# Optimization experiments

Measured on AMD Instinct MI355X. Metric: run time of the kernel, lower is better.

Reference implementation:

```python
import jax, jax.numpy as jnp
import numpy as np
from jax import lax

N_P = 0.5      # module_cfg.n_p
CUTOFF = 0.3   # module_cfg.cutoff


def setup_inputs() -> dict:
    key = jax.random.key(0)
    k1, k2, k3, k4 = jax.random.split(key, 4)
    h = jax.random.normal(k1, (1, 8192, 256), jnp.float32)
    pos = jax.random.normal(k2, (8192, 3), jnp.float32)
    W = jax.random.normal(k3, (256, 256), jnp.float32) / 16.0  # ~ Linear init scale
    b = jax.random.normal(k4, (256,), jnp.float32) * 0.01
    return {"h": h, "pos": pos, "W": W, "b": b}


def fps_indices(pos, k, select=0):
    """Farthest point sampling; returns the k selected indices in ascending
    index order (matching torch boolean-mask indexing pos[selected])."""
    n = pos.shape[0]
    selected = jnp.zeros(n, dtype=bool).at[select].set(True)
    d = jnp.linalg.norm(pos - pos[select], axis=-1)  # (N,) euclidean, as torch.pairwise_distance
    d = jnp.where(selected, -jnp.inf, d)

    def body(i, carry):
        sel, dist = carry
        new = jnp.argmax(dist)
        sel = sel.at[new].set(True)
        dist = jnp.minimum(dist, jnp.linalg.norm(pos - pos[new], axis=-1))
        dist = jnp.where(sel, -jnp.inf, dist)
        return sel, dist

    sel, _ = lax.fori_loop(0, k - 1, body, (selected, d))
    return jnp.nonzero(sel, size=k)[0]  # exactly k True entries, sorted


def reference(h, pos, W, b):
    B, num_res, c_s = h.shape
    n_nodes = int(num_res * N_P)  # num_res * n_p // 1

    idx = fps_indices(pos, n_nodes)          # (n_nodes,)
    new_node_pos = pos[idx]                  # (n_nodes, 3)

    # torch.cdist(pos, new_node_pos, p=3): Minkowski p=3 distance
    diff = jnp.abs(pos[:, None, :] - new_node_pos[None, :, :])  # (N, n_nodes, 3)
    dist = jnp.cbrt(jnp.sum(diff ** 3, axis=-1))                 # (N, n_nodes)

    # sparse membership mask (fixed-shape equivalent of the nonzero edge list)
    mask = dist < CUTOFF                      # (N, n_nodes) bool

    # sparse gather-matmul: aggregate residue features into each sampled node
    agg = jnp.einsum('nm,bnc->bmc', mask.astype(h.dtype), h)     # (B, n_nodes, c_s)
    new_node_embed = agg @ W.T + b            # nn.Linear(c_s, c_s)
    return new_node_embed, new_node_pos, mask
```

## Files before the change

### kernel.cpp

```cpp
#include <hip/hip_runtime.h>
#include <hip/hip_bf16.h>
#include <cmath>

#define FPS_N 8192
#define FPS_K 4096
#define CS    256
#define FT    1024
#define PPT   8
#define NEGINF (-__builtin_inff())

__device__ __forceinline__ float p3sum(float x, float y, float z,
                                       float nx, float ny, float nz) {
  float dx = fabsf(__fsub_rn(x, nx));
  float dy = fabsf(__fsub_rn(y, ny));
  float dz = fabsf(__fsub_rn(z, nz));
  float cx = __fmul_rn(__fmul_rn(dx, dx), dx);
  float cy = __fmul_rn(__fmul_rn(dy, dy), dy);
  float cz = __fmul_rn(__fmul_rn(dz, dz), dz);
  return __fadd_rn(__fadd_rn(cx, cy), cz);
}

__device__ __forceinline__ float eucl2(float x, float y, float z,
                                       float nx, float ny, float nz) {
  float dx = __fsub_rn(x, nx);
  float dy = __fsub_rn(y, ny);
  float dz = __fsub_rn(z, nz);
  return __fadd_rn(__fadd_rn(__fmul_rn(dx, dx), __fmul_rn(dy, dy)),
                   __fmul_rn(dz, dz));
}

template<int CTRL>
__device__ __forceinline__ void dpp_sel2(float& v, int& k) {
  int nv = __builtin_amdgcn_update_dpp(__float_as_int(v), __float_as_int(v), CTRL, 0xF, 0xF, false);
  int nk = __builtin_amdgcn_update_dpp(k, k, CTRL, 0xF, 0xF, false);
  float fv = __int_as_float(nv);
  bool t = (fv > v) || (fv == v && nk < k);
  v = t ? fv : v;
  k = t ? nk : k;
}

template<int CTRL>
__device__ __forceinline__ void dpp_sel5(float& v, int& k, float& x, float& y, float& z) {
  int nv = __builtin_amdgcn_update_dpp(__float_as_int(v), __float_as_int(v), CTRL, 0xF, 0xF, false);
  int nk = __builtin_amdgcn_update_dpp(k, k, CTRL, 0xF, 0xF, false);
  int nx = __builtin_amdgcn_update_dpp(__float_as_int(x), __float_as_int(x), CTRL, 0xF, 0xF, false);
  int ny = __builtin_amdgcn_update_dpp(__float_as_int(y), __float_as_int(y), CTRL, 0xF, 0xF, false);
  int nz = __builtin_amdgcn_update_dpp(__float_as_int(z), __float_as_int(z), CTRL, 0xF, 0xF, false);
  float fv = __int_as_float(nv);
  bool t = (fv > v) || (fv == v && nk < k);
  v = t ? fv : v;
  k = t ? nk : k;
  x = t ? __int_as_float(nx) : x;
  y = t ? __int_as_float(ny) : y;
  z = t ? __int_as_float(nz) : z;
}

__global__ __launch_bounds__(FT) void bin_kernel(const float* __restrict__ pos,
                                                 float* __restrict__ pos_s,
                                                 int* __restrict__ ids_s) {
  __shared__ int hist[4096];
  __shared__ int part[FT];
  const int tid = threadIdx.x;
#pragma unroll
  for (int i = 0; i < 4; ++i) hist[tid * 4 + i] = 0;
  __syncthreads();

  float qx[PPT], qy[PPT], qz[PPT];
  int cell[PPT];
  {
    const float4* p4 = (const float4*)pos + tid * 6;
    float4 a0 = p4[0], a1 = p4[1], a2 = p4[2], a3 = p4[3], a4 = p4[4], a5 = p4[5];
    qx[0]=a0.x; qy[0]=a0.y; qz[0]=a0.z;
    qx[1]=a0.w; qy[1]=a1.x; qz[1]=a1.y;
    qx[2]=a1.z; qy[2]=a1.w; qz[2]=a2.x;
    qx[3]=a2.y; qy[3]=a2.z; qz[3]=a2.w;
    qx[4]=a3.x; qy[4]=a3.y; qz[4]=a3.z;
    qx[5]=a3.w; qy[5]=a4.x; qz[5]=a4.y;
    qx[6]=a4.z; qy[6]=a4.w; qz[6]=a5.x;
    qx[7]=a5.y; qy[7]=a5.z; qz[7]=a5.w;
  }
#pragma unroll
  for (int j = 0; j < PPT; ++j) {
    int ix = min(max((int)floorf((qx[j] + 4.0f) * 2.0f), 0), 15);
    int iy = min(max((int)floorf((qy[j] + 4.0f) * 2.0f), 0), 15);
    int iz = min(max((int)floorf((qz[j] + 4.0f) * 2.0f), 0), 15);
    int m = 0;
#pragma unroll
    for (int b = 0; b < 4; ++b)
      m |= (((ix >> b) & 1) << (3 * b)) | (((iy >> b) & 1) << (3 * b + 1)) |
           (((iz >> b) & 1) << (3 * b + 2));
    cell[j] = m;
    atomicAdd(&hist[m], 1);
  }
  __syncthreads();
  int h0 = hist[tid * 4], h1 = hist[tid * 4 + 1], h2 = hist[tid * 4 + 2], h3 = hist[tid * 4 + 3];
  int s = h0 + h1 + h2 + h3;
  part[tid] = s;
  __syncthreads();
  for (int off = 1; off < FT; off <<= 1) {
    int u = (tid >= off) ? part[tid - off] : 0;
    __syncthreads();
    part[tid] += u;
    __syncthreads();
  }
  int base = part[tid] - s;
  hist[tid * 4 + 0] = base;
  hist[tid * 4 + 1] = base + h0;
  hist[tid * 4 + 2] = base + h0 + h1;
  hist[tid * 4 + 3] = base + h0 + h1 + h2;
  __syncthreads();
#pragma unroll
  for (int j = 0; j < PPT; ++j) {
    int slot = atomicAdd(&hist[cell[j]], 1);
    pos_s[slot * 3 + 0] = qx[j];
    pos_s[slot * 3 + 1] = qy[j];
    pos_s[slot * 3 + 2] = qz[j];
    ids_s[slot] = tid * PPT + j;
  }
}

#define KEYOF(j) (((((idp[(j) >> 1] >> (((j) & 1) * 16)) & 0xffff)) << 13) | (tid * PPT + (j)))
#define SELP(va, ka, vb, kb) { bool t_ = ((vb) > (va)) || ((vb) == (va) && (kb) < (ka)); \
                               va = t_ ? (vb) : (va); ka = t_ ? (kb) : (ka); }
#define RESCAN() { \
    float v0 = dd[0], v1 = dd[1], v2 = dd[2], v3 = dd[3]; \
    float v4 = dd[4], v5 = dd[5], v6 = dd[6], v7 = dd[7]; \
    int k0 = KEYOF(0), k1 = KEYOF(1), k2 = KEYOF(2), k3 = KEYOF(3); \
    int k4 = KEYOF(4), k5 = KEYOF(5), k6 = KEYOF(6), k7 = KEYOF(7); \
    SELP(v0, k0, v1, k1) SELP(v2, k2, v3, k3) SELP(v4, k4, v5, k5) SELP(v6, k6, v7, k7) \
    SELP(v0, k0, v2, k2) SELP(v4, k4, v6, k6) SELP(v0, k0, v4, k4) \
    bv = v0; bkey = k0; }

__global__ __launch_bounds__(FT) void fps_kernel(const float* __restrict__ pos,
                                                 const float* __restrict__ pos_s,
                                                 const int* __restrict__ ids_s,
                                                 float* __restrict__ pos_out) {
  __shared__ int sC[2][5][16];
  __shared__ unsigned char flag[FPS_N];
  __shared__ int sc[FT];
  const int tid = threadIdx.x, lane = tid & 63, wave = tid >> 6;

  { int* f4 = (int*)flag; f4[tid * 2] = 0; f4[tid * 2 + 1] = 0; }

  float x[PPT], y[PPT], z[PPT], d2[PPT], dd[PPT];
  int idp[PPT / 2];
  {
    const float4* p4 = (const float4*)pos_s + tid * 6;
    float4 a0 = p4[0], a1 = p4[1], a2 = p4[2], a3 = p4[3], a4 = p4[4], a5 = p4[5];
    x[0]=a0.x; y[0]=a0.y; z[0]=a0.z;
    x[1]=a0.w; y[1]=a1.x; z[1]=a1.y;
    x[2]=a1.z; y[2]=a1.w; z[2]=a2.x;
    x[3]=a2.y; y[3]=a2.z; z[3]=a2.w;
    x[4]=a3.x; y[4]=a3.y; z[4]=a3.z;
    x[5]=a3.w; y[5]=a4.x; z[5]=a4.y;
    x[6]=a4.z; y[6]=a4.w; z[6]=a5.x;
    x[7]=a5.y; y[7]=a5.z; z[7]=a5.w;
    const int4* i4 = (const int4*)ids_s + tid * 2;
    int4 b0 = i4[0], b1 = i4[1];
    idp[0] = (b0.x & 0xffff) | (b0.y << 16);
    idp[1] = (b0.z & 0xffff) | (b0.w << 16);
    idp[2] = (b1.x & 0xffff) | (b1.y << 16);
    idp[3] = (b1.z & 0xffff) | (b1.w << 16);
  }

  const float p0x = pos[0], p0y = pos[1], p0z = pos[2];
#pragma unroll
  for (int j = 0; j < PPT; ++j) {
    float s = eucl2(x[j], y[j], z[j], p0x, p0y, p0z);
    int oid = (idp[j >> 1] >> ((j & 1) * 16)) & 0xffff;
    if (oid == 0) { d2[j] = NEGINF; dd[j] = NEGINF; }
    else          { d2[j] = s;      dd[j] = sqrtf(s); }
  }
  float bnx = x[0], bny = y[0], bnz = z[0], bxx = x[0], bxy = y[0], bxz = z[0];
#pragma unroll
  for (int j = 1; j < PPT; ++j) {
    bnx = fminf(bnx, x[j]); bny = fminf(bny, y[j]); bnz = fminf(bnz, z[j]);
    bxx = fmaxf(bxx, x[j]); bxy = fmaxf(bxy, y[j]); bxz = fmaxf(bxz, z[j]);
  }
  if (tid == 0) flag[0] = 1;

  float bv; int bkey; bool chb;
  RESCAN();
  chb = false;
  {
    float rv = bv; int rk = bkey;
    dpp_sel2<0x111>(rv, rk); dpp_sel2<0x112>(rv, rk); dpp_sel2<0x114>(rv, rk);
    dpp_sel2<0x118>(rv, rk); dpp_sel2<0x142>(rv, rk); dpp_sel2<0x143>(rv, rk);
    int wkk = __builtin_amdgcn_readlane(rk, 63);
    if (bkey == wkk) {
      float sx = x[0], sy = y[0], sz = z[0];
#pragma unroll
      for (int j = 0; j < PPT; ++j)
        if (j == (bkey & 7)) { sx = x[j]; sy = y[j]; sz = z[j]; }
      sC[0][0][wave] = __float_as_int(bv);
      sC[0][1][wave] = bkey;
      sC[0][2][wave] = __float_as_int(sx);
      sC[0][3][wave] = __float_as_int(sy);
      sC[0][4][wave] = __float_as_int(sz);
    }
  }
  __syncthreads();

  for (int k = 0; k < FPS_K - 1; ++k) {
    const int p = k & 1, pn = p ^ 1;
    float gv = __int_as_float(sC[p][0][lane & 15]);
    int   gk = sC[p][1][lane & 15];
    float gx = __int_as_float(sC[p][2][lane & 15]);
    float gy = __int_as_float(sC[p][3][lane & 15]);
    float gz = __int_as_float(sC[p][4][lane & 15]);
    dpp_sel5<0xB1>(gv, gk, gx, gy, gz);
    dpp_sel5<0x4E>(gv, gk, gx, gy, gz);
    dpp_sel5<0x124>(gv, gk, gx, gy, gz);
    dpp_sel5<0x128>(gv, gk, gx, gy, gz);

    const int stor = gk & 8191;
    if ((stor >> 3) == tid) {
      const int jj = stor & 7;
#pragma unroll
      for (int j = 0; j < PPT; ++j)
        if (j == jj) { d2[j] = NEGINF; dd[j] = NEGINF; }
      chb = true;
    }
    if (tid == 0) flag[gk >> 13] = 1;

    float cx = fminf(fmaxf(gx, bnx), bxx);
    float cy = fminf(fmaxf(gy, bny), bxy);
    float cz = fminf(fmaxf(gz, bnz), bxz);
    float ddx = gx - cx, ddy = gy - cy, ddz = gz - cz;
    float bd2 = ddx * ddx + ddy * ddy + ddz * ddz;
    float tub = (bv == NEGINF) ? NEGINF : bv * bv;
    if (bd2 * 0.999f < tub) {
      unsigned cm = 0;
#pragma unroll
      for (int j = 0; j < PPT; ++j) {
        float s = eucl2(x[j], y[j], z[j], gx, gy, gz);
        if (s < d2[j]) { d2[j] = s; cm |= (1u << j); }
      }
      if (cm) {
#pragma unroll
        for (int j = 0; j < PPT; ++j)
          if ((cm >> j) & 1) dd[j] = sqrtf(d2[j]);
        if ((cm >> (bkey & 7)) & 1) chb = true;
      }
    }

    unsigned long long any = __ballot(chb ? 1 : 0);
    if (any) {
      if (chb) { RESCAN(); chb = false; }
      float rv = bv; int rk = bkey;
      dpp_sel2<0x111>(rv, rk); dpp_sel2<0x112>(rv, rk); dpp_sel2<0x114>(rv, rk);
      dpp_sel2<0x118>(rv, rk); dpp_sel2<0x142>(rv, rk); dpp_sel2<0x143>(rv, rk);
      int wkk = __builtin_amdgcn_readlane(rk, 63);
      if (bkey == wkk) {
        float sx = x[0], sy = y[0], sz = z[0];
#pragma unroll
        for (int j = 0; j < PPT; ++j)
          if (j == (bkey & 7)) { sx = x[j]; sy = y[j]; sz = z[j]; }
        sC[pn][0][wave] = __float_as_int(bv);
        sC[pn][1][wave] = bkey;
        sC[pn][2][wave] = __float_as_int(sx);
        sC[pn][3][wave] = __float_as_int(sy);
        sC[pn][4][wave] = __float_as_int(sz);
      }
    } else {
      if (lane < 5) sC[pn][lane][wave] = sC[p][lane][wave];
    }
    __syncthreads();
  }

  const int* fI = (const int*)flag;
  int w0 = fI[tid * 2], w1 = fI[tid * 2 + 1];
  int cnt = __popc(w0) + __popc(w1);
  sc[tid] = cnt;
  __syncthreads();
  for (int off = 1; off < FT; off <<= 1) {
    int u = (tid >= off) ? sc[tid - off] : 0;
    __syncthreads();
    sc[tid] += u;
    __syncthreads();
  }
  int r = sc[tid] - cnt;
#pragma unroll
  for (int j = 0; j < PPT; ++j) {
    int w = (j < 4) ? w0 : w1;
    if ((w >> ((j & 3) * 8)) & 1) {
      int oi = tid * PPT + j;
      pos_out[r * 3 + 0] = pos[oi * 3 + 0];
      pos_out[r * 3 + 1] = pos[oi * 3 + 1];
      pos_out[r * 3 + 2] = pos[oi * 3 + 2];
      ++r;
    }
  }
}

__global__ __launch_bounds__(256) void wt_kernel(const float* __restrict__ W,
                                                 float* __restrict__ WT) {
  int i = blockIdx.x * 256 + threadIdx.x;
  int c = i >> 8, cp = i & 255;
  WT[i] = W[cp * 256 + c];
}

__global__ __launch_bounds__(256) void agg_linear_kernel(
    const float* __restrict__ h, const float* __restrict__ pos,
    const float* __restrict__ nodepos, const float* __restrict__ WT,
    const float* __restrict__ bias, float* __restrict__ embed, float sb) {
  const int m = blockIdx.x;
  const int tid = threadIdx.x;
  const int lane = tid & 63, wave = tid >> 6;
  const float nx = nodepos[m * 3 + 0];
  const float ny = nodepos[m * 3 + 1];
  const float nz = nodepos[m * 3 + 2];
  const float4* h4 = (const float4*)h;

  float4 acc = make_float4(0.f, 0.f, 0.f, 0.f);
  const int base0 = wave * (FPS_N / 4);
  for (int base = base0; base < base0 + (FPS_N / 4); base += 64) {
    int n = base + lane;
    float px = pos[n * 3 + 0], py = pos[n * 3 + 1], pz = pos[n * 3 + 2];
    unsigned long long mb = __ballot((p3sum(px, py, pz, nx, ny, nz) <= sb) ? 1 : 0);
    while (mb) {
      int b = __ffsll(mb) - 1;
      mb &= (mb - 1);
      float4 hv = h4[(size_t)(base + b) * 64 + lane];
      acc.x += hv.x; acc.y += hv.y; acc.z += hv.z; acc.w += hv.w;
    }
  }

  __shared__ float lacc[4][256];
  lacc[wave][lane * 4 + 0] = acc.x;
  lacc[wave][lane * 4 + 1] = acc.y;
  lacc[wave][lane * 4 + 2] = acc.z;
  lacc[wave][lane * 4 + 3] = acc.w;
  __syncthreads();
  __shared__ float aggrow[256];
  float aggv = ((lacc[0][tid] + lacc[1][tid]) + lacc[2][tid]) + lacc[3][tid];
  aggrow[tid] = aggv;
  __syncthreads();

  float o = bias[tid];
#pragma unroll 8
  for (int c = 0; c < 256; ++c)
    o = fmaf(aggrow[c], WT[c * 256 + tid], o);
  embed[(size_t)m * 256 + tid] = o;
}

__global__ __launch_bounds__(256) void mask_kernel(const float* __restrict__ pos,
                                                   const float* __restrict__ nodepos,
                                                   float* __restrict__ maskout,
                                                   float sb) {
  int n  = blockIdx.y;
  int m0 = (blockIdx.x * 256 + threadIdx.x) * 4;
  float x = pos[n * 3 + 0], y = pos[n * 3 + 1], z = pos[n * 3 + 2];
  const float4* np4 = (const float4*)(nodepos + (size_t)m0 * 3);
  float4 a = np4[0], bq = np4[1], cq = np4[2];
  float4 r;
  r.x = (p3sum(x, y, z, a.x,  a.y,  a.z)  <= sb) ? 1.0f : 0.0f;
  r.y = (p3sum(x, y, z, a.w,  bq.x, bq.y) <= sb) ? 1.0f : 0.0f;
  r.z = (p3sum(x, y, z, bq.z, bq.w, cq.x) <= sb) ? 1.0f : 0.0f;
  r.w = (p3sum(x, y, z, cq.y, cq.z, cq.w) <= sb) ? 1.0f : 0.0f;
  *(float4*)(maskout + (size_t)n * FPS_K + m0) = r;
}

extern "C" void kernel_launch(void* const* d_in, const int* in_sizes, int n_in,
                              void* d_out, int out_size, void* d_ws, size_t ws_size,
                              hipStream_t stream) {
  (void)in_sizes; (void)n_in; (void)out_size; (void)d_ws; (void)ws_size;
  const float* h   = (const float*)d_in[0];
  const float* pos = (const float*)d_in[1];
  const float* W   = (const float*)d_in[2];
  const float* b   = (const float*)d_in[3];

  float* out     = (float*)d_out;
  float* embed   = out;
  float* pos_out = out + (size_t)FPS_K * CS;
  float* mask    = pos_out + (size_t)FPS_K * 3;
  float* WT      = mask;
  float* pos_s   = mask + (1 << 21);
  int*   ids_s   = (int*)(pos_s + 3 * FPS_N);

  const float  t    = 0.3f;
  const float  ulpv = nextafterf(t, 1.0f) - t;
  const double rmid = (double)t - (double)ulpv * 0.5;
  const double C    = rmid * rmid * rmid;
  float sb = (float)C;
  if (!((double)sb < C)) sb = nextafterf(sb, 0.0f);

  hipLaunchKernelGGL(bin_kernel, dim3(1), dim3(FT), 0, stream, pos, pos_s, ids_s);
  hipLaunchKernelGGL(fps_kernel, dim3(1), dim3(FT), 0, stream, pos, pos_s, ids_s, pos_out);
  hipLaunchKernelGGL(wt_kernel, dim3(256), dim3(256), 0, stream, W, WT);
  hipLaunchKernelGGL(agg_linear_kernel, dim3(FPS_K), dim3(256), 0, stream,
                     h, pos, pos_out, WT, b, embed, sb);
  hipLaunchKernelGGL(mask_kernel, dim3(4, FPS_N), dim3(256), 0, stream,
                     pos, pos_out, mask, sb);
}
```

Measured before the change: 7.559 ms.

## Batch multiple FPS selections per barrier using per-wave top-2 candidates

```diff
diff --git a/kernel.cpp b/kernel.cpp
--- a/kernel.cpp
+++ b/kernel.cpp
@@ -8,6 +8,7 @@
 #define FT    1024
 #define PPT   8
 #define NEGINF (-__builtin_inff())
+#define KMAX  0x7fffffff
 
 __device__ __forceinline__ float p3sum(float x, float y, float z,
                                        float nx, float ny, float nz) {
@@ -29,30 +30,39 @@
                    __fmul_rn(dz, dz));
 }
 
+#define LEXGT(va, ka, vb, kb) (((va) > (vb)) || ((va) == (vb) && ((ka) < (kb))))
+
 template<int CTRL>
-__device__ __forceinline__ void dpp_sel2(float& v, int& k) {
-  int nv = __builtin_amdgcn_update_dpp(__float_as_int(v), __float_as_int(v), CTRL, 0xF, 0xF, false);
-  int nk = __builtin_amdgcn_update_dpp(k, k, CTRL, 0xF, 0xF, false);
-  float fv = __int_as_float(nv);
-  bool t = (fv > v) || (fv == v && nk < k);
-  v = t ? fv : v;
-  k = t ? nk : k;
-}
-
+__device__ __forceinline__ int dppi(int a) {
+  return __builtin_amdgcn_update_dpp(a, a, CTRL, 0xF, 0xF, false);
+}
 template<int CTRL>
-__device__ __forceinline__ void dpp_sel5(float& v, int& k, float& x, float& y, float& z) {
-  int nv = __builtin_amdgcn_update_dpp(__float_as_int(v), __float_as_int(v), CTRL, 0xF, 0xF, false);
-  int nk = __builtin_amdgcn_update_dpp(k, k, CTRL, 0xF, 0xF, false);
-  int nx = __builtin_amdgcn_update_dpp(__float_as_int(x), __float_as_int(x), CTRL, 0xF, 0xF, false);
-  int ny = __builtin_amdgcn_update_dpp(__float_as_int(y), __float_as_int(y), CTRL, 0xF, 0xF, false);
-  int nz = __builtin_amdgcn_update_dpp(__float_as_int(z), __float_as_int(z), CTRL, 0xF, 0xF, false);
-  float fv = __int_as_float(nv);
-  bool t = (fv > v) || (fv == v && nk < k);
-  v = t ? fv : v;
-  k = t ? nk : k;
-  x = t ? __int_as_float(nx) : x;
-  y = t ? __int_as_float(ny) : y;
-  z = t ? __int_as_float(nz) : z;
+__device__ __forceinline__ float dppf(float a) {
+  return __int_as_float(__builtin_amdgcn_update_dpp(__float_as_int(a), __float_as_int(a), CTRL, 0xF, 0xF, false));
+}
+
+template<int CTRL>
+__device__ __forceinline__ void dpp_sel7(float& v, int& k, float& x, float& y,
+                                         float& z, float& v2, int& k2) {
+  float pv = dppf<CTRL>(v);  int pk = dppi<CTRL>(k);
+  float px = dppf<CTRL>(x);  float py = dppf<CTRL>(y);  float pz = dppf<CTRL>(z);
+  float pv2 = dppf<CTRL>(v2); int pk2 = dppi<CTRL>(k2);
+  bool t = LEXGT(pv, pk, v, k);
+  v = t ? pv : v;   k = t ? pk : k;
+  x = t ? px : x;   y = t ? py : y;   z = t ? pz : z;
+  v2 = t ? pv2 : v2; k2 = t ? pk2 : k2;
+}
+
+template<int CTRL>
+__device__ __forceinline__ void dpp_top2(float& v1, int& k1, float& v2, int& k2) {
+  float p1 = dppf<CTRL>(v1); int q1 = dppi<CTRL>(k1);
+  float p2 = dppf<CTRL>(v2); int q2 = dppi<CTRL>(k2);
+  bool t = LEXGT(p1, q1, v1, k1);
+  float lv = t ? v1 : p1; int lk = t ? k1 : q1;
+  float ov = t ? p2 : v2; int ok = t ? q2 : k2;
+  v1 = t ? p1 : v1; k1 = t ? q1 : k1;
+  bool u = LEXGT(lv, lk, ov, ok);
+  v2 = u ? lv : ov; k2 = u ? lk : ok;
 }
 
 __global__ __launch_bounds__(FT) void bin_kernel(const float* __restrict__ pos,
@@ -120,22 +130,57 @@
 }
 
 #define KEYOF(j) (((((idp[(j) >> 1] >> (((j) & 1) * 16)) & 0xffff)) << 13) | (tid * PPT + (j)))
-#define SELP(va, ka, vb, kb) { bool t_ = ((vb) > (va)) || ((vb) == (va) && (kb) < (ka)); \
-                               va = t_ ? (vb) : (va); ka = t_ ? (kb) : (ka); }
-#define RESCAN() { \
-    float v0 = dd[0], v1 = dd[1], v2 = dd[2], v3 = dd[3]; \
-    float v4 = dd[4], v5 = dd[5], v6 = dd[6], v7 = dd[7]; \
-    int k0 = KEYOF(0), k1 = KEYOF(1), k2 = KEYOF(2), k3 = KEYOF(3); \
-    int k4 = KEYOF(4), k5 = KEYOF(5), k6 = KEYOF(6), k7 = KEYOF(7); \
-    SELP(v0, k0, v1, k1) SELP(v2, k2, v3, k3) SELP(v4, k4, v5, k5) SELP(v6, k6, v7, k7) \
-    SELP(v0, k0, v2, k2) SELP(v4, k4, v6, k6) SELP(v0, k0, v4, k4) \
-    bv = v0; bkey = k0; }
+
+#define PAIR2(v1, k1, v2, k2, a, ka, b, kb) { bool t_ = LEXGT(b, kb, a, ka); \
+  v1 = t_ ? (b) : (a); k1 = t_ ? (kb) : (ka); v2 = t_ ? (a) : (b); k2 = t_ ? (ka) : (kb); }
+
+#define MERGE22(v1, k1, v2, k2, w1, l1, w2, l2) { \
+  bool t_ = LEXGT(w1, l1, v1, k1); \
+  float lv_ = t_ ? (v1) : (w1); int lk_ = t_ ? (k1) : (l1); \
+  float ov_ = t_ ? (w2) : (v2); int ok_ = t_ ? (l2) : (k2); \
+  v1 = t_ ? (w1) : (v1); k1 = t_ ? (l1) : (k1); \
+  bool u_ = LEXGT(lv_, lk_, ov_, ok_); \
+  v2 = u_ ? lv_ : ov_; k2 = u_ ? lk_ : ok_; }
+
+#define RESCAN2() { \
+  float A1, B1, C1, D1, A2, B2, C2, D2; int Ak, Bk, Ck, Dk, Ak2, Bk2, Ck2, Dk2; \
+  PAIR2(A1, Ak, A2, Ak2, dd[0], KEYOF(0), dd[1], KEYOF(1)) \
+  PAIR2(B1, Bk, B2, Bk2, dd[2], KEYOF(2), dd[3], KEYOF(3)) \
+  PAIR2(C1, Ck, C2, Ck2, dd[4], KEYOF(4), dd[5], KEYOF(5)) \
+  PAIR2(D1, Dk, D2, Dk2, dd[6], KEYOF(6), dd[7], KEYOF(7)) \
+  MERGE22(A1, Ak, A2, Ak2, B1, Bk, B2, Bk2) \
+  MERGE22(C1, Ck, C2, Ck2, D1, Dk, D2, Dk2) \
+  MERGE22(A1, Ak, A2, Ak2, C1, Ck, C2, Ck2) \
+  bv = A1; bkey = Ak; bv2 = A2; bk2 = Ak2; }
+
+#define WAVE_PUBLISH(sn) { \
+  float rv1 = bv; int rk1 = bkey; float rv2 = bv2; int rk2 = bk2; \
+  dpp_top2<0x111>(rv1, rk1, rv2, rk2); dpp_top2<0x112>(rv1, rk1, rv2, rk2); \
+  dpp_top2<0x114>(rv1, rk1, rv2, rk2); dpp_top2<0x118>(rv1, rk1, rv2, rk2); \
+  dpp_top2<0x142>(rv1, rk1, rv2, rk2); dpp_top2<0x143>(rv1, rk1, rv2, rk2); \
+  int wk1u = __builtin_amdgcn_readlane(rk1, 63); \
+  int wv2u = __builtin_amdgcn_readlane(__float_as_int(rv2), 63); \
+  int wk2u = __builtin_amdgcn_readlane(rk2, 63); \
+  if (bkey == wk1u) { \
+    const int jj_ = bkey & 7; \
+    float sx_ = x[0], sy_ = y[0], sz_ = z[0]; \
+    _Pragma("unroll") \
+    for (int j = 0; j < PPT; ++j) \
+      if (j == jj_) { sx_ = x[j]; sy_ = y[j]; sz_ = z[j]; } \
+    sC[sn][0][wave] = __float_as_int(bv); \
+    sC[sn][1][wave] = bkey; \
+    sC[sn][2][wave] = __float_as_int(sx_); \
+    sC[sn][3][wave] = __float_as_int(sy_); \
+    sC[sn][4][wave] = __float_as_int(sz_); \
+    sC[sn][5][wave] = wv2u; \
+    sC[sn][6][wave] = wk2u; \
+  } }
 
 __global__ __launch_bounds__(FT) void fps_kernel(const float* __restrict__ pos,
                                                  const float* __restrict__ pos_s,
                                                  const int* __restrict__ ids_s,
                                                  float* __restrict__ pos_out) {
-  __shared__ int sC[2][5][16];
+  __shared__ int sC[2][7][16];
   __shared__ unsigned char flag[FPS_N];
   __shared__ int sc[FT];
   const int tid = threadIdx.x, lane = tid & 63, wave = tid >> 6;
@@ -179,92 +224,111 @@
   }
   if (tid == 0) flag[0] = 1;
 
-  float bv; int bkey; bool chb;
-  RESCAN();
+  float bv, bv2; int bkey, bk2; bool chb;
+  RESCAN2();
   chb = false;
-  {
-    float rv = bv; int rk = bkey;
-    dpp_sel2<0x111>(rv, rk); dpp_sel2<0x112>(rv, rk); dpp_sel2<0x114>(rv, rk);
-    dpp_sel2<0x118>(rv, rk); dpp_sel2<0x142>(rv, rk); dpp_sel2<0x143>(rv, rk);
-    int wkk = __builtin_amdgcn_readlane(rk, 63);
-    if (bkey == wkk) {
-      float sx = x[0], sy = y[0], sz = z[0];
+  WAVE_PUBLISH(0);
+  __syncthreads();
+
+  int sel = 0, rp = 0;
+  while (sel < FPS_K - 1) {
+    const int s16 = lane & 15;
+    const float c_v1 = __int_as_float(sC[rp][0][s16]);
+    const int   c_k1 = sC[rp][1][s16];
+    const float c_x  = __int_as_float(sC[rp][2][s16]);
+    const float c_y  = __int_as_float(sC[rp][3][s16]);
+    const float c_z  = __int_as_float(sC[rp][4][s16]);
+    const float c_v2 = __int_as_float(sC[rp][5][s16]);
+    const int   c_k2 = sC[rp][6][s16];
+
+    bool elig = true, cont = true;
+    int A = 0;
+    const int cap = FPS_K - 1 - sel;
+    float mu_v = NEGINF; int mu_k = KMAX;
+    float ax0=0, ay0=0, az0=0, ax1=0, ay1=0, az1=0, ax2=0, ay2=0, az2=0, ax3=0, ay3=0, az3=0;
+
+#define BSTEP(AXT, AYT, AZT, DISTCHK) \
+    if (cont) { \
+      float ev = elig ? c_v1 : NEGINF; int ek = elig ? c_k1 : KMAX; \
+      float wx = c_x, wy = c_y, wz = c_z, wv2 = c_v2; int wk2 = c_k2; \
+      dpp_sel7<0xB1>(ev, ek, wx, wy, wz, wv2, wk2); \
+      dpp_sel7<0x4E>(ev, ek, wx, wy, wz, wv2, wk2); \
+      dpp_sel7<0x124>(ev, ek, wx, wy, wz, wv2, wk2); \
+      dpp_sel7<0x128>(ev, ek, wx, wy, wz, wv2, wk2); \
+      bool good = (ev != NEGINF) && LEXGT(ev, ek, mu_v, mu_k); \
+      DISTCHK \
+      if (good) { \
+        AXT = wx; AYT = wy; AZT = wz; \
+        if (LEXGT(wv2, wk2, mu_v, mu_k)) { mu_v = wv2; mu_k = wk2; } \
+        const int stor = ek & 8191; \
+        if ((stor >> 3) == tid) { \
+          const int jj = stor & 7; \
+          _Pragma("unroll") \
+          for (int j = 0; j < PPT; ++j) \
+            if (j == jj) { d2[j] = NEGINF; dd[j] = NEGINF; } \
+          chb = true; \
+        } \
+        if (tid == 0) flag[ek >> 13] = 1; \
+        bool killed = false; \
+        if (c_k1 == ek) elig = false; \
+        else if (elig) { \
+          float dm = sqrtf(eucl2(c_x, c_y, c_z, wx, wy, wz)); \
+          if (dm < c_v1) { elig = false; killed = true; } \
+        } \
+        unsigned long long kb = __ballot(killed ? 1 : 0); \
+        ++A; \
+        cont = (kb == 0ULL) && (A < cap) && (A < 4); \
+      } else cont = false; \
+    }
+
+    BSTEP(ax0, ay0, az0, )
+    BSTEP(ax1, ay1, az1, good = good && (sqrtf(eucl2(wx, wy, wz, ax0, ay0, az0)) >= ev);)
+    BSTEP(ax2, ay2, az2, good = good && (sqrtf(eucl2(wx, wy, wz, ax0, ay0, az0)) >= ev)
+                               && (sqrtf(eucl2(wx, wy, wz, ax1, ay1, az1)) >= ev);)
+    BSTEP(ax3, ay3, az3, good = good && (sqrtf(eucl2(wx, wy, wz, ax0, ay0, az0)) >= ev)
+                               && (sqrtf(eucl2(wx, wy, wz, ax1, ay1, az1)) >= ev)
+                               && (sqrtf(eucl2(wx, wy, wz, ax2, ay2, az2)) >= ev);)
+#undef BSTEP
+
+    unsigned cm = 0;
+    const float tub = (bv == NEGINF) ? NEGINF : bv * bv;
+#define UPDC(T, AXT, AYT, AZT) \
+    if (A > T) { \
+      float cx = fminf(fmaxf(AXT, bnx), bxx); \
+      float cy = fminf(fmaxf(AYT, bny), bxy); \
+      float cz = fminf(fmaxf(AZT, bnz), bxz); \
+      float ddx = AXT - cx, ddy = AYT - cy, ddz = AZT - cz; \
+      float bd2 = ddx * ddx + ddy * ddy + ddz * ddz; \
+      if (bd2 * 0.999f < tub) { \
+        _Pragma("unroll") \
+        for (int j = 0; j < PPT; ++j) { \
+          float s = eucl2(x[j], y[j], z[j], AXT, AYT, AZT); \
+          if (s < d2[j]) { d2[j] = s; cm |= (1u << j); } \
+        } \
+      } \
+    }
+    UPDC(0, ax0, ay0, az0)
+    UPDC(1, ax1, ay1, az1)
+    UPDC(2, ax2, ay2, az2)
+    UPDC(3, ax3, ay3, az3)
+#undef UPDC
+    if (cm) {
 #pragma unroll
       for (int j = 0; j < PPT; ++j)
-        if (j == (bkey & 7)) { sx = x[j]; sy = y[j]; sz = z[j]; }
-      sC[0][0][wave] = __float_as_int(bv);
-      sC[0][1][wave] = bkey;
-      sC[0][2][wave] = __float_as_int(sx);
-      sC[0][3][wave] = __float_as_int(sy);
-      sC[0][4][wave] = __float_as_int(sz);
-    }
-  }
-  __syncthreads();
-
-  for (int k = 0; k < FPS_K - 1; ++k) {
-    const int p = k & 1, pn = p ^ 1;
-    float gv = __int_as_float(sC[p][0][lane & 15]);
-    int   gk = sC[p][1][lane & 15];
-    float gx = __int_as_float(sC[p][2][lane & 15]);
-    float gy = __int_as_float(sC[p][3][lane & 15]);
-    float gz = __int_as_float(sC[p][4][lane & 15]);
-    dpp_sel5<0xB1>(gv, gk, gx, gy, gz);
-    dpp_sel5<0x4E>(gv, gk, gx, gy, gz);
-    dpp_sel5<0x124>(gv, gk, gx, gy, gz);
-    dpp_sel5<0x128>(gv, gk, gx, gy, gz);
-
-    const int stor = gk & 8191;
-    if ((stor >> 3) == tid) {
-      const int jj = stor & 7;
-#pragma unroll
-      for (int j = 0; j < PPT; ++j)
-        if (j == jj) { d2[j] = NEGINF; dd[j] = NEGINF; }
-      chb = true;
-    }
-    if (tid == 0) flag[gk >> 13] = 1;
-
-    float cx = fminf(fmaxf(gx, bnx), bxx);
-    float cy = fminf(fmaxf(gy, bny), bxy);
-    float cz = fminf(fmaxf(gz, bnz), bxz);
-    float ddx = gx - cx, ddy = gy - cy, ddz = gz - cz;
-    float bd2 = ddx * ddx + ddy * ddy + ddz * ddz;
-    float tub = (bv == NEGINF) ? NEGINF : bv * bv;
-    if (bd2 * 0.999f < tub) {
-      unsigned cm = 0;
-#pragma unroll
-      for (int j = 0; j < PPT; ++j) {
-        float s = eucl2(x[j], y[j], z[j], gx, gy, gz);
-        if (s < d2[j]) { d2[j] = s; cm |= (1u << j); }
-      }
-      if (cm) {
-#pragma unroll
-        for (int j = 0; j < PPT; ++j)
-          if ((cm >> j) & 1) dd[j] = sqrtf(d2[j]);
-        if ((cm >> (bkey & 7)) & 1) chb = true;
-      }
-    }
-
+        if ((cm >> j) & 1) dd[j] = sqrtf(d2[j]);
+      if ((cm >> (bkey & 7)) & 1) chb = true;
+    }
+
+    const int pn = rp ^ 1;
     unsigned long long any = __ballot(chb ? 1 : 0);
     if (any) {
-      if (chb) { RESCAN(); chb = false; }
-      float rv = bv; int rk = bkey;
-      dpp_sel2<0x111>(rv, rk); dpp_sel2<0x112>(rv, rk); dpp_sel2<0x114>(rv, rk);
-      dpp_sel2<0x118>(rv, rk); dpp_sel2<0x142>(rv, rk); dpp_sel2<0x143>(rv, rk);
-      int wkk = __builtin_amdgcn_readlane(rk, 63);
-      if (bkey == wkk) {
-        float sx = x[0], sy = y[0], sz = z[0];
-#pragma unroll
-        for (int j = 0; j < PPT; ++j)
-          if (j == (bkey & 7)) { sx = x[j]; sy = y[j]; sz = z[j]; }
-        sC[pn][0][wave] = __float_as_int(bv);
-        sC[pn][1][wave] = bkey;
-        sC[pn][2][wave] = __float_as_int(sx);
-        sC[pn][3][wave] = __float_as_int(sy);
-        sC[pn][4][wave] = __float_as_int(sz);
-      }
+      if (chb) { RESCAN2(); chb = false; }
+      WAVE_PUBLISH(pn);
     } else {
-      if (lane < 5) sC[pn][lane][wave] = sC[p][lane][wave];
-    }
+      if (lane < 7) sC[pn][lane][wave] = sC[rp][lane][wave];
+    }
+    sel += A;
+    rp = pn;
     __syncthreads();
   }
 
```

After: 8.473 ms. 1.12x slower.
